# Kernel optimization log

Measured on AMD Instinct MI355X. Metric: run time of the kernel, lower is better.

The kernel has to match this reference:

```python
import jax, jax.numpy as jnp
import numpy as np

N, E, B = 20000, 320000, 64
HID, DEPTH, NFREQ = 128, 4, 8
NODE_DIM, EDGE_DIM, SG = 4, 3, 230
TWO_PI = 2.0 * np.pi


def setup_inputs() -> dict:
    key = jax.random.key(0)
    ks = jax.random.split(key, 20)
    inp = {}
    inp["x"] = jax.random.normal(ks[0], (N, NODE_DIM), jnp.float32)
    inp["edge_index"] = jax.random.randint(ks[1], (2, E), 0, N)
    inp["edge_attr"] = jax.random.normal(ks[2], (E, EDGE_DIM), jnp.float32)
    inp["batch"] = jnp.sort(jax.random.randint(ks[3], (N,), 0, B))
    inp["space_group"] = jax.random.randint(ks[4], (B,), 0, SG)
    inp["node_w"] = jax.random.normal(ks[5], (NODE_DIM, HID), jnp.float32) * 0.1
    inp["node_b"] = jnp.zeros((HID,), jnp.float32)
    inp["sg_table"] = jax.random.normal(ks[6], (SG, HID), jnp.float32) * 0.1
    inp["lin_w"] = jax.random.normal(ks[7], (DEPTH, 2 * HID + EDGE_DIM, HID), jnp.float32) * 0.05
    inp["lin_b"] = jnp.zeros((DEPTH, HID), jnp.float32)
    inp["att_w"] = jax.random.normal(ks[8], (DEPTH, 2 * HID + EDGE_DIM), jnp.float32) * 0.05
    inp["att_b"] = jnp.zeros((DEPTH,), jnp.float32)
    inp["fk_w"] = jax.random.normal(ks[9], (DEPTH, NFREQ, HID, HID), jnp.float32) * 0.1
    inp["fk_b"] = jnp.zeros((DEPTH, HID), jnp.float32)
    inp["bn_g"] = jnp.ones((DEPTH, HID), jnp.float32)
    inp["bn_b"] = jnp.zeros((DEPTH, HID), jnp.float32)
    inp["pool_w"] = jax.random.normal(ks[10], (HID,), jnp.float32) * 0.1
    inp["pool_b"] = jnp.zeros((), jnp.float32)
    inp["head_w1"] = jax.random.normal(ks[11], (4, 2 * HID, HID), jnp.float32) * 0.05
    inp["head_b1"] = jnp.zeros((4, HID), jnp.float32)
    for i, (nm, od) in enumerate([("e", 1), ("s", 3), ("c", 7), ("m", 3)]):
        inp[nm + "_w2"] = jax.random.normal(ks[12 + i], (HID, od), jnp.float32) * 0.05
        inp[nm + "_b2"] = jnp.zeros((od,), jnp.float32)
    return inp


def reference(x, edge_index, edge_attr, batch, space_group, node_w, node_b, sg_table,
              lin_w, lin_b, att_w, att_b, fk_w, fk_b, bn_g, bn_b, pool_w, pool_b,
              head_w1, head_b1, e_w2, e_b2, s_w2, s_b2, c_w2, c_b2, m_w2, m_b2):
    src, dst = edge_index[0], edge_index[1]  # x_j = x[src], x_i = x[dst]
    h = x @ node_w + node_b                  # [N, HID]
    sg = sg_table[space_group]               # [B, HID]
    freqs = jnp.arange(1, NFREQ + 1, dtype=h.dtype)
    for l in range(DEPTH):
        # edge conv: gather-concat-linear-sigmoid attention-scatter add
        tmp = jnp.concatenate([h[dst], h[src], edge_attr], axis=-1)   # [E, 2H+3]
        alpha = jax.nn.sigmoid(tmp @ att_w[l] + att_b[l])[:, None]    # [E, 1]
        msg = alpha * (tmp @ lin_w[l] + lin_b[l])                     # [E, H]
        h_conv = jax.ops.segment_sum(msg, dst, num_segments=N)
        # Fourier-Kolmogorov branch
        ang = TWO_PI * freqs[None, :, None] * h[:, None, :]           # [N, K, H]
        h_fk = (jnp.einsum('nki,kio->no', jnp.sin(ang), fk_w[l])
                + jnp.einsum('nki,kio->no', jnp.cos(ang), fk_w[l]) + fk_b[l])
        h = h_conv + h_fk
        # BatchNorm1d (batch statistics, training semantics) + ReLU; dropout = identity (eval)
        mu = h.mean(axis=0)
        var = h.var(axis=0)
        h = (h - mu) / jnp.sqrt(var + 1e-5) * bn_g[l] + bn_b[l]
        h = jax.nn.relu(h)
    # attention pool: softmax over ALL nodes (dim=0), as in the original
    a = jax.nn.softmax(h @ pool_w + pool_b, axis=0)[:, None]          # [N, 1]
    pooled = jax.ops.segment_sum(a * h, batch, num_segments=B)        # [B, H]
    comb = jnp.concatenate([pooled, sg], axis=-1)                     # [B, 2H]

    def head(i, w2, b2):
        z = jax.nn.relu(comb @ head_w1[i] + head_b1[i])
        return z @ w2 + b2

    energy = head(0, e_w2, e_b2)          # [B, 1]
    stability = head(1, s_w2, s_b2)       # [B, 3]
    crystal_system = head(2, c_w2, c_b2)  # [B, 7]
    material_type = head(3, m_w2, m_b2)   # [B, 3]
    return energy, stability, crystal_system, material_type
```

## Files before the change

### kernel.cpp

```cpp
#include <hip/hip_runtime.h>
#include <math.h>

#define HID 128
#define DEPTH 4
#define PSPLIT 16
#define SMAXB 40

typedef _Float16 half8 __attribute__((ext_vector_type(8)));
typedef float f4 __attribute__((ext_vector_type(4)));

__global__ void k_node_embed(const float* __restrict__ x, const float* __restrict__ nw,
                             const float* __restrict__ nb, float* __restrict__ h, int N) {
    int idx = blockIdx.x * blockDim.x + threadIdx.x;
    if (idx >= N * HID) return;
    int n = idx >> 7, c = idx & 127;
    float acc = nb[c];
#pragma unroll
    for (int d = 0; d < 4; ++d) acc += x[n * 4 + d] * nw[d * HID + c];
    h[idx] = acc;
}

__global__ void k_wsplit(const float* __restrict__ fkw, _Float16* __restrict__ whi,
                         _Float16* __restrict__ wlo) {
    __shared__ float sh[64][65];
    int bid = blockIdx.x;
    int l = bid >> 5; int r = bid & 31; int kb = r >> 1; int nbk = r & 1;
    const float* W = fkw + (size_t)l * 131072;
    _Float16* Hl = whi + (size_t)l * 131072;
    _Float16* Ll = wlo + (size_t)l * 131072;
    int k0 = kb * 64, n0 = nbk * 64;
    for (int i = threadIdx.x; i < 4096; i += 256) {
        int kk = i >> 6, nn = i & 63;
        sh[kk][nn] = W[(k0 + kk) * HID + n0 + nn];
    }
    __syncthreads();
    for (int i = threadIdx.x; i < 4096; i += 256) {
        int nn = i >> 6, kk = i & 63;
        float w = sh[kk][nn];
        _Float16 hi = (_Float16)w;
        _Float16 lo = (_Float16)((w - (float)hi) * 2048.f);
        Hl[(n0 + nn) * 1024 + k0 + kk] = hi;
        Ll[(n0 + nn) * 1024 + k0 + kk] = lo;
    }
}

__global__ void k_hist(const int* __restrict__ dst, int* __restrict__ deg, int E) {
    int e = blockIdx.x * 256 + threadIdx.x;
    if (e < E) atomicAdd(&deg[dst[e]], 1);
}

__global__ void k_scan_a(const int* __restrict__ deg, int* __restrict__ bsum, int N) {
    __shared__ int sh[256];
    int i = blockIdx.x * 256 + threadIdx.x;
    sh[threadIdx.x] = (i < N) ? deg[i] : 0;
    __syncthreads();
    for (int off = 128; off > 0; off >>= 1) {
        if (threadIdx.x < (unsigned)off) sh[threadIdx.x] += sh[threadIdx.x + off];
        __syncthreads();
    }
    if (threadIdx.x == 0) bsum[blockIdx.x] = sh[0];
}

__global__ void k_scan_b(int* __restrict__ bsum, int nb) {
    __shared__ int sh[256];
    int v = (threadIdx.x < (unsigned)nb) ? bsum[threadIdx.x] : 0;
    sh[threadIdx.x] = v;
    __syncthreads();
    for (int off = 1; off < 256; off <<= 1) {
        int add = (threadIdx.x >= (unsigned)off) ? sh[threadIdx.x - off] : 0;
        __syncthreads();
        sh[threadIdx.x] += add;
        __syncthreads();
    }
    if (threadIdx.x < (unsigned)nb) bsum[threadIdx.x] = sh[threadIdx.x] - v;
}

__global__ void k_scan_c(const int* __restrict__ deg, const int* __restrict__ bsum,
                         int* __restrict__ offs, int* __restrict__ cursor, int N) {
    __shared__ int sh[256];
    int i = blockIdx.x * 256 + threadIdx.x;
    int v = (i < N) ? deg[i] : 0;
    sh[threadIdx.x] = v;
    __syncthreads();
    for (int off = 1; off < 256; off <<= 1) {
        int add = (threadIdx.x >= (unsigned)off) ? sh[threadIdx.x - off] : 0;
        __syncthreads();
        sh[threadIdx.x] += add;
        __syncthreads();
    }
    int ex = bsum[blockIdx.x] + sh[threadIdx.x] - v;
    if (i < N) { offs[i] = ex; cursor[i] = ex; }
    if (i == N - 1) offs[N] = ex + v;
}

__global__ void k_scatter(const int* __restrict__ src, const int* __restrict__ dst,
                          const float* __restrict__ ea, int* cursor,
                          int* __restrict__ srco, float4* __restrict__ ea3o, int E) {
    int e = blockIdx.x * 256 + threadIdx.x;
    if (e < E) {
        int d = dst[e];
        int p = atomicAdd(&cursor[d], 1);
        srco[p] = src[e];
        float4 q;
        q.x = ea[e * 3 + 0]; q.y = ea[e * 3 + 1]; q.z = ea[e * 3 + 2]; q.w = 0.f;
        ea3o[p] = q;
    }
}

__global__ void k_bstart(const int* __restrict__ batch, int* __restrict__ boffs, int N, int B) {
    int n = blockIdx.x * 256 + threadIdx.x;
    if (n >= N) return;
    int b1 = batch[n];
    if (n == 0) for (int b = 0; b <= b1; ++b) boffs[b] = 0;
    int b2 = (n + 1 < N) ? batch[n + 1] : B;
    for (int b = b1 + 1; b <= b2; ++b) boffs[b] = n + 1;
}

__global__ __launch_bounds__(256) void k_node_lin(const float* __restrict__ h,
                           const float* __restrict__ linw, const float* __restrict__ linb,
                           const float* __restrict__ attw, const float* __restrict__ attb,
                           float* __restrict__ A1, float* __restrict__ A2,
                           float* __restrict__ a1, float* __restrict__ a2, int N) {
    __shared__ float hT[HID][20];
    int nb = blockIdx.x * 16;
    int tid = threadIdx.x;
    for (int i = tid; i < 16 * HID; i += 256) {
        int n = i >> 7, c = i & 127;
        int gn = nb + n;
        hT[c][n] = (gn < N) ? h[gn * HID + c] : 0.f;
    }
    __syncthreads();
    {
        int node = tid >> 4, lane16 = tid & 15;
        float p1 = 0.f, p2 = 0.f;
#pragma unroll
        for (int j = 0; j < 8; ++j) {
            int k = lane16 * 8 + j;
            float hv = hT[k][node];
            p1 += hv * attw[k];
            p2 += hv * attw[128 + k];
        }
        for (int off = 8; off > 0; off >>= 1) {
            p1 += __shfl_down(p1, off, 16);
            p2 += __shfl_down(p2, off, 16);
        }
        int gn = nb + node;
        if (lane16 == 0 && gn < N) {
            a1[gn] = p1 + attb[0];
            a2[gn] = p2;
        }
    }
    int c = tid & 127, r = tid >> 7;
    const float* Wd = linw;
    const float* Ws = linw + 128 * HID;
    float acc1[8] = {0, 0, 0, 0, 0, 0, 0, 0}, acc2[8] = {0, 0, 0, 0, 0, 0, 0, 0};
#pragma unroll 4
    for (int k = 0; k < HID; ++k) {
        float wd = Wd[k * HID + c];
        float ws = Ws[k * HID + c];
        float4 h0 = *(const float4*)&hT[k][r * 8];
        float4 h1 = *(const float4*)&hT[k][r * 8 + 4];
        acc1[0] += h0.x * wd; acc2[0] += h0.x * ws;
        acc1[1] += h0.y * wd; acc2[1] += h0.y * ws;
        acc1[2] += h0.z * wd; acc2[2] += h0.z * ws;
        acc1[3] += h0.w * wd; acc2[3] += h0.w * ws;
        acc1[4] += h1.x * wd; acc2[4] += h1.x * ws;
        acc1[5] += h1.y * wd; acc2[5] += h1.y * ws;
        acc1[6] += h1.z * wd; acc2[6] += h1.z * ws;
        acc1[7] += h1.w * wd; acc2[7] += h1.w * ws;
    }
    float lb = linb[c];
#pragma unroll
    for (int j = 0; j < 8; ++j) {
        int gn = nb + r * 8 + j;
        if (gn < N) {
            A1[(size_t)gn * HID + c] = acc1[j] + lb;
            A2[(size_t)gn * HID + c] = acc2[j];
        }
    }
}

__global__ __launch_bounds__(256) void k_edge(const float* __restrict__ A1,
        const float* __restrict__ A2, const float* __restrict__ a1,
        const float* __restrict__ a2, const int* __restrict__ srco,
        const float4* __restrict__ ea3o, const int* __restrict__ offs,
        const float* __restrict__ linw3, const float* __restrict__ attw3,
        float* __restrict__ hconv, double* __restrict__ stats, int N) {
    __shared__ float part[8][HID + 4];
    int n = blockIdx.x;
    int tid = threadIdx.x;
    if (n == 0) stats[tid] = 0.0;
    int lane32 = tid & 31, slot = tid >> 5;
    int c4 = lane32 * 4;
    float4 w0v = *(const float4*)&linw3[c4];
    float4 w1v = *(const float4*)&linw3[HID + c4];
    float4 w2v = *(const float4*)&linw3[2 * HID + c4];
    float aw0 = attw3[0], aw1 = attw3[1], aw2 = attw3[2];
    float a1n = a1[n];
    float4 A1v = *(const float4*)&A1[(size_t)n * HID + c4];
    float4 acc; acc.x = acc.y = acc.z = acc.w = 0.f;
    int s0 = offs[n], s1 = offs[n + 1];
    for (int idx = s0 + slot; idx < s1; idx += 8) {
        int s = srco[idx];
        float4 q = ea3o[idx];
        float logit = a1n + a2[s] + q.x * aw0 + q.y * aw1 + q.z * aw2;
        float al = 1.f / (1.f + __expf(-logit));
        float4 a2v = *(const float4*)&A2[(size_t)s * HID + c4];
        float4 pre;
        pre.x = A1v.x + a2v.x + q.x * w0v.x + q.y * w1v.x + q.z * w2v.x;
        pre.y = A1v.y + a2v.y + q.x * w0v.y + q.y * w1v.y + q.z * w2v.y;
        pre.z = A1v.z + a2v.z + q.x * w0v.z + q.y * w1v.z + q.z * w2v.z;
        pre.w = A1v.w + a2v.w + q.x * w0v.w + q.y * w1v.w + q.z * w2v.w;
        acc.x += al * pre.x; acc.y += al * pre.y;
        acc.z += al * pre.z; acc.w += al * pre.w;
    }
    *(float4*)&part[slot][c4] = acc;
    __syncthreads();
    if (slot == 0) {
        float4 p = *(const float4*)&part[0][c4];
#pragma unroll
        for (int s = 1; s < 8; ++s) {
            float4 r = *(const float4*)&part[s][c4];
            p.x += r.x; p.y += r.y; p.z += r.z; p.w += r.w;
        }
        *(float4*)&hconv[(size_t)n * HID + c4] = p;
    }
}

#define FK_ROWS 32
__global__ __launch_bounds__(512, 4) void k_fk(const float* __restrict__ h,
        const _Float16* __restrict__ whi, const _Float16* __restrict__ wlo,
        float* __restrict__ p0, float* __restrict__ p1, int N) {
    __shared__ _Float16 ahi[FK_ROWS * 256];
    __shared__ _Float16 alo[FK_ROWS * 256];
    int tid = threadIdx.x;
    int bx = blockIdx.x;
    int nb = (bx >> 1) * FK_ROWS;
    int ks = bx & 1;
    int row = tid >> 4;
    int o16 = tid & 15;
    {
    }
    int gn = nb + row;
    int rc = (gn < N) ? gn : (N - 1);
    const float* hp = h + (size_t)rc * HID + o16 * 8;
    float hv[8];
    *(float4*)&hv[0] = *(const float4*)hp;
    *(float4*)&hv[4] = *(const float4*)(hp + 4);
    int rs = row & 7;
    int lane = tid & 63, wv = tid >> 6;
    int quad = lane >> 4, l16 = lane & 15;
    int n0w = wv * 16;
    int rs16 = (l16 & 7) << 3;
    f4 acc0[2], accL[2];
#pragma unroll
    for (int mi = 0; mi < 2; ++mi) { acc0[mi] = (f4)(0.f); accL[mi] = (f4)(0.f); }
    int kbase0 = ks * 512;
#pragma unroll
    for (int chunk = 0; chunk < 2; ++chunk) {
        int kbase = kbase0 + chunk * 256;
        int fr0 = kbase >> 7;
#pragma unroll
        for (int g = 0; g < 2; ++g) {
            float freqf = 6.2831853f * (float)(fr0 + g + 1);
            half8 vh, vl;
#pragma unroll
            for (int j = 0; j < 8; ++j) {
                float ang = freqf * hv[j] + 0.78539816f;
                float a = 1.41421356f * __sinf(ang);
                _Float16 hi = (_Float16)a;
                vh[j] = hi;
                vl[j] = (_Float16)((a - (float)hi) * 2048.f);
            }
            int oct = (g * 16 + o16) ^ rs;
            *(half8*)&ahi[row * 256 + oct * 8] = vh;
            *(half8*)&alo[row * 256 + oct * 8] = vl;
        }
        __syncthreads();
        const _Float16* bhp = whi + (size_t)(n0w + l16) * 1024 + kbase + quad * 8;
        const _Float16* blp = wlo + (size_t)(n0w + l16) * 1024 + kbase + quad * 8;
#pragma unroll 2
        for (int step = 0; step < 8; ++step) {
            int ka = (step * 32 + quad * 8) ^ rs16;
            int ko = step * 32;
            half8 bh = *(const half8*)(bhp + ko);
            half8 bl = *(const half8*)(blp + ko);
            half8 ah[2], al[2];
#pragma unroll
            for (int mi = 0; mi < 2; ++mi) {
                ah[mi] = *(const half8*)&ahi[(l16 + mi * 16) * 256 + ka];
                al[mi] = *(const half8*)&alo[(l16 + mi * 16) * 256 + ka];
            }
#pragma unroll
            for (int mi = 0; mi < 2; ++mi) {
                acc0[mi] = __builtin_amdgcn_mfma_f32_16x16x32_f16(ah[mi], bh, acc0[mi], 0, 0, 0);
                accL[mi] = __builtin_amdgcn_mfma_f32_16x16x32_f16(ah[mi], bl, accL[mi], 0, 0, 0);
                accL[mi] = __builtin_amdgcn_mfma_f32_16x16x32_f16(al[mi], bh, accL[mi], 0, 0, 0);
            }
        }
        __syncthreads();
    }
    float* p = ks ? p1 : p0;
    const float inv = 1.0f / 2048.0f;
#pragma unroll
    for (int mi = 0; mi < 2; ++mi)
#pragma unroll
        for (int r = 0; r < 4; ++r) {
            int g2 = nb + mi * 16 + quad * 4 + r;
            if (g2 < N)
                p[g2 * HID + n0w + l16] = acc0[mi][r] + accL[mi][r] * inv;
        }
}

__global__ __launch_bounds__(256) void k_bn_stats(float* __restrict__ hconv,
                           const float* __restrict__ p0, const float* __restrict__ p1,
                           const float* __restrict__ fkb,
                           double* __restrict__ stats, int N) {
    int tid = threadIdx.x;
    int cq = tid & 31, rg = tid >> 5;
    int c4 = cq * 4;
    float4 bias = *(const float4*)&fkb[c4];
    float s1[4] = {0, 0, 0, 0}, s2[4] = {0, 0, 0, 0};
    for (int n = blockIdx.x * 8 + rg; n < N; n += gridDim.x * 8) {
        size_t idx = (size_t)n * HID + c4;
        float4 a  = *(const float4*)&hconv[idx];
        float4 b0 = *(const float4*)&p0[idx];
        float4 b1 = *(const float4*)&p1[idx];
        float4 v;
        v.x = a.x + b0.x + b1.x + bias.x;
        v.y = a.y + b0.y + b1.y + bias.y;
        v.z = a.z + b0.z + b1.z + bias.z;
        v.w = a.w + b0.w + b1.w + bias.w;
        *(float4*)&hconv[idx] = v;
        s1[0] += v.x; s2[0] += v.x * v.x;
        s1[1] += v.y; s2[1] += v.y * v.y;
        s1[2] += v.z; s2[2] += v.z * v.z;
        s1[3] += v.w; s2[3] += v.w * v.w;
    }
#pragma unroll
    for (int j = 0; j < 4; ++j) {
        s1[j] += __shfl_down(s1[j], 32);
        s2[j] += __shfl_down(s2[j], 32);
    }
    __shared__ float sh1[4][32][4], sh2[4][32][4];
    int wv = tid >> 6, lane = tid & 63;
    if (lane < 32) {
#pragma unroll
        for (int j = 0; j < 4; ++j) { sh1[wv][lane][j] = s1[j]; sh2[wv][lane][j] = s2[j]; }
    }
    __syncthreads();
    if (tid < 128) {
        int cq2 = tid >> 2, j2 = tid & 3;
        float t1 = sh1[0][cq2][j2] + sh1[1][cq2][j2] + sh1[2][cq2][j2] + sh1[3][cq2][j2];
        float t2 = sh2[0][cq2][j2] + sh2[1][cq2][j2] + sh2[2][cq2][j2] + sh2[3][cq2][j2];
        int c = cq2 * 4 + j2;
        atomicAdd(&stats[c], (double)t1);
        atomicAdd(&stats[128 + c], (double)t2);
    }
}

__global__ void k_bn_apply(const float* __restrict__ hsum, const double* __restrict__ stats,
                           const float* __restrict__ g, const float* __restrict__ b,
                           const float* __restrict__ pw, const float* __restrict__ pb,
                           float* __restrict__ h, float* __restrict__ s,
                           int do_score, int N) {
    int idx = blockIdx.x * 256 + threadIdx.x;
    int row = idx >> 5, cq = idx & 31;
    int c4 = cq * 4;
    int valid = row < N;
    double invN = 1.0 / (double)N;
    float p = 0.f;
    if (valid) {
        float4 hv = *(const float4*)&hsum[(size_t)row * HID + c4];
        float vin[4] = {hv.x, hv.y, hv.z, hv.w};
        float4 ov;
        float* po = &ov.x;
#pragma unroll
        for (int j = 0; j < 4; ++j) {
            int c = c4 + j;
            float mu = (float)(stats[c] * invN);
            float var = (float)(stats[128 + c] * invN) - mu * mu;
            float inv = 1.f / sqrtf(var + 1e-5f);
            float sc = g[c] * inv;
            float sh = b[c] - mu * sc;
            float oo = fmaxf(vin[j] * sc + sh, 0.f);
            po[j] = oo;
            if (do_score) p += oo * pw[c];
        }
        *(float4*)&h[(size_t)row * HID + c4] = ov;
    }
    if (do_score) {
        for (int off = 16; off > 0; off >>= 1) p += __shfl_down(p, off, 32);
        if ((threadIdx.x & 31) == 0 && valid) s[row] = p + pb[0];
    }
}

__global__ void k_smax1(const float* __restrict__ s, float* __restrict__ mzp, int N) {
    __shared__ float red[256];
    float m = -INFINITY;
    for (int n = blockIdx.x * 256 + threadIdx.x; n < N; n += SMAXB * 256)
        m = fmaxf(m, s[n]);
    red[threadIdx.x] = m;
    __syncthreads();
    for (int off = 128; off > 0; off >>= 1) {
        if (threadIdx.x < (unsigned)off)
            red[threadIdx.x] = fmaxf(red[threadIdx.x], red[threadIdx.x + off]);
        __syncthreads();
    }
    m = red[0];
    __syncthreads();
    float z = 0.f;
    for (int n = blockIdx.x * 256 + threadIdx.x; n < N; n += SMAXB * 256)
        z += __expf(s[n] - m);
    red[threadIdx.x] = z;
    __syncthreads();
    for (int off = 128; off > 0; off >>= 1) {
        if (threadIdx.x < (unsigned)off) red[threadIdx.x] += red[threadIdx.x + off];
        __syncthreads();
    }
    if (threadIdx.x == 0) { mzp[blockIdx.x * 2] = m; mzp[blockIdx.x * 2 + 1] = red[0]; }
}

__device__ __forceinline__ void combine_mz(const float* mzp, float& m, float& Z) {
    m = -INFINITY;
#pragma unroll 8
    for (int i = 0; i < SMAXB; ++i) m = fmaxf(m, mzp[i * 2]);
    Z = 0.f;
#pragma unroll 8
    for (int i = 0; i < SMAXB; ++i) Z += mzp[i * 2 + 1] * __expf(mzp[i * 2] - m);
}

__global__ void k_pool_part(const float* __restrict__ h, const float* __restrict__ s,
                            const float* __restrict__ mzp, const int* __restrict__ boffs,
                            float* __restrict__ part) {
    int b = blockIdx.x >> 4, split = blockIdx.x & (PSPLIT - 1);
    int c = threadIdx.x & 127, half = threadIdx.x >> 7;
    float m, Z;
    combine_mz(mzp, m, Z);
    (void)Z;
    int n0 = boffs[b], n1 = boffs[b + 1];
    float acc = 0.f;
    for (int n = n0 + split * 2 + half; n < n1; n += PSPLIT * 2)
        acc += __expf(s[n] - m) * h[n * HID + c];
    __shared__ float prt[2][HID];
    prt[half][c] = acc;
    __syncthreads();
    if (half == 0) part[(size_t)(b * PSPLIT + split) * HID + c] = prt[0][c] + prt[1][c];
}

__global__ void k_pool_sum(const float* __restrict__ part, const float* __restrict__ mzp,
                           float* __restrict__ pooled) {
    int b = blockIdx.x, c = threadIdx.x;
    float m, Z;
    combine_mz(mzp, m, Z);
    float acc = 0.f;
#pragma unroll
    for (int i = 0; i < PSPLIT; ++i) acc += part[(size_t)(b * PSPLIT + i) * HID + c];
    pooled[b * HID + c] = acc / Z;
}

__global__ __launch_bounds__(256) void k_head(const float* __restrict__ pooled,
                       const float* __restrict__ sg_table,
                       const int* __restrict__ space_group,
                       const float* __restrict__ hw1, const float* __restrict__ hb1,
                       const float* __restrict__ ew2, const float* __restrict__ eb2,
                       const float* __restrict__ sw2, const float* __restrict__ sb2,
                       const float* __restrict__ cw2, const float* __restrict__ cb2,
                       const float* __restrict__ mw2, const float* __restrict__ mb2,
                       float* __restrict__ out, int B) {
    __shared__ float comb[256];
    __shared__ float zred[2][128];
    __shared__ float zsh[128];
    int b = blockIdx.x >> 2, i = blockIdx.x & 3;
    int t = threadIdx.x;
    comb[t] = (t < 128) ? pooled[b * HID + t] : sg_table[space_group[b] * HID + (t - 128)];
    __syncthreads();
    int half = t >> 7, tt = t & 127;
    const float* W = hw1 + ((size_t)i * 256 + half * 128) * HID;
    const float* cb = &comb[half * 128];
    float z = 0.f;
#pragma unroll 8
    for (int k = 0; k < 128; ++k) z += cb[k] * W[k * HID + tt];
    zred[half][tt] = z;
    __syncthreads();
    if (t < 128) zsh[t] = fmaxf(zred[0][t] + zred[1][t] + hb1[i * HID + t], 0.f);
    __syncthreads();
    const int od[4] = {1, 3, 7, 3};
    const int base[4] = {0, 64, 256, 704};
    const float* w2 = (i == 0) ? ew2 : (i == 1) ? sw2 : (i == 2) ? cw2 : mw2;
    const float* b2 = (i == 0) ? eb2 : (i == 1) ? sb2 : (i == 2) ? cb2 : mb2;
    int odi = od[i];
    if (t < odi) {
        float o = b2[t];
        for (int c = 0; c < HID; ++c) o += zsh[c] * w2[c * odi + t];
        out[base[i] + b * odi + t] = o;
    }
}

extern "C" void kernel_launch(void* const* d_in, const int* in_sizes, int n_in,
                              void* d_out, int out_size, void* d_ws, size_t ws_size,
                              hipStream_t stream) {
    const float* x          = (const float*)d_in[0];
    const int*   edge_index = (const int*)d_in[1];
    const float* edge_attr  = (const float*)d_in[2];
    const int*   batch      = (const int*)d_in[3];
    const int*   space_group= (const int*)d_in[4];
    const float* node_w     = (const float*)d_in[5];
    const float* node_b     = (const float*)d_in[6];
    const float* sg_table   = (const float*)d_in[7];
    const float* lin_w      = (const float*)d_in[8];
    const float* lin_b      = (const float*)d_in[9];
    const float* att_w      = (const float*)d_in[10];
    const float* att_b      = (const float*)d_in[11];
    const float* fk_w       = (const float*)d_in[12];
    const float* fk_b       = (const float*)d_in[13];
    const float* bn_g       = (const float*)d_in[14];
    const float* bn_b       = (const float*)d_in[15];
    const float* pool_w     = (const float*)d_in[16];
    const float* pool_b     = (const float*)d_in[17];
    const float* head_w1    = (const float*)d_in[18];
    const float* head_b1    = (const float*)d_in[19];
    const float* ew2 = (const float*)d_in[20]; const float* eb2 = (const float*)d_in[21];
    const float* sw2 = (const float*)d_in[22]; const float* sb2 = (const float*)d_in[23];
    const float* cw2 = (const float*)d_in[24]; const float* cb2 = (const float*)d_in[25];
    const float* mw2 = (const float*)d_in[26]; const float* mb2 = (const float*)d_in[27];
    float* out = (float*)d_out;

    const int N = in_sizes[3];
    const int E = in_sizes[1] / 2;
    const int B = in_sizes[4];
    const int* src = edge_index;
    const int* dst = edge_index + E;

    char* w = (char*)d_ws;
    auto alloc = [&](size_t bytes) { char* p = w; w += (bytes + 255) & ~(size_t)255; return p; };
    float*  h      = (float*)alloc((size_t)N * HID * 4);
    float*  A1     = (float*)alloc((size_t)N * HID * 4);
    float*  A2     = (float*)alloc((size_t)N * HID * 4);
    float*  hconv  = (float*)alloc((size_t)N * HID * 4);
    float*  a1     = (float*)alloc((size_t)N * 4);
    float*  a2     = (float*)alloc((size_t)N * 4);
    float*  sbuf   = (float*)alloc((size_t)N * 4);
    int*    deg    = (int*)alloc((size_t)N * 4);
    int*    cursor = (int*)alloc((size_t)N * 4);
    int*    offs   = (int*)alloc((size_t)(N + 1) * 4);
    int*    srco   = (int*)alloc((size_t)E * 4);
    float4* ea3o   = (float4*)alloc((size_t)E * 16);
    _Float16* whi  = (_Float16*)alloc((size_t)DEPTH * 1024 * HID * 2);
    _Float16* wlo  = (_Float16*)alloc((size_t)DEPTH * 1024 * HID * 2);
    int*    bsum   = (int*)alloc(256 * 4);
    int*    boffs  = (int*)alloc((size_t)(B + 1) * 4);
    double* stats  = (double*)alloc(256 * 8);
    float*  mzp    = (float*)alloc(SMAXB * 2 * 4);
    float*  part   = (float*)alloc((size_t)B * PSPLIT * HID * 4);
    float*  pooled = (float*)alloc((size_t)B * HID * 4);

    const int nchunk = (N + 255) / 256;
    const int echunk = (E + 255) / 256;

    k_wsplit<<<128, 256, 0, stream>>>(fk_w, whi, wlo);
    hipMemsetAsync(deg, 0, (size_t)N * 4, stream);
    k_hist<<<echunk, 256, 0, stream>>>(dst, deg, E);
    k_scan_a<<<nchunk, 256, 0, stream>>>(deg, bsum, N);
    k_scan_b<<<1, 256, 0, stream>>>(bsum, nchunk);
    k_scan_c<<<nchunk, 256, 0, stream>>>(deg, bsum, offs, cursor, N);
    k_scatter<<<echunk, 256, 0, stream>>>(src, dst, edge_attr, cursor, srco, ea3o, E);
    k_bstart<<<nchunk, 256, 0, stream>>>(batch, boffs, N, B);

    k_node_embed<<<(N * HID + 255) / 256, 256, 0, stream>>>(x, node_w, node_b, h, N);

    for (int l = 0; l < DEPTH; ++l) {
        const float* linw_l = lin_w + (size_t)l * 259 * HID;
        k_node_lin<<<(N + 15) / 16, 256, 0, stream>>>(
            h, linw_l, lin_b + l * HID, att_w + (size_t)l * 259, att_b + l,
            A1, A2, a1, a2, N);
        k_edge<<<N, 256, 0, stream>>>(A1, A2, a1, a2, srco, ea3o, offs,
                                      linw_l + 256 * HID, att_w + (size_t)l * 259 + 256,
                                      hconv, stats, N);
        k_fk<<<((N + FK_ROWS - 1) / FK_ROWS) * 2, 512, 0, stream>>>(
            h, whi + (size_t)l * 131072, wlo + (size_t)l * 131072, A1, A2, N);
        k_bn_stats<<<320, 256, 0, stream>>>(hconv, A1, A2, fk_b + l * HID, stats, N);
        k_bn_apply<<<(N * 32 + 255) / 256, 256, 0, stream>>>(
            hconv, stats, bn_g + l * HID, bn_b + l * HID, pool_w, pool_b,
            h, sbuf, (l == DEPTH - 1) ? 1 : 0, N);
    }

    k_smax1<<<SMAXB, 256, 0, stream>>>(sbuf, mzp, N);
    k_pool_part<<<B * PSPLIT, 256, 0, stream>>>(h, sbuf, mzp, boffs, part);
    k_pool_sum<<<B, 128, 0, stream>>>(part, mzp, pooled);
    k_head<<<B * 4, 256, 0, stream>>>(pooled, sg_table, space_group, head_w1, head_b1,
                                      ew2, eb2, sw2, sb2, cw2, cb2, mw2, mb2, out, B);
}
```

Before: 709.8 us.

## Merge k-split fk blocks into one double-buffered pipelined kernel

Each k_fk block now processes the full K=1024 reduction instead of two blocks writing separate partial outputs. The sin/cos activation tile for the next chunk is generated into a second LDS buffer while MFMAs consume the current one. This removes one partial buffer's global write and read in the BN stats kernel and overlaps trig with matrix math. It doubles LDS per block and halves the grid, which may lower occupancy and parallelism.

```diff
diff --git a/kernel.cpp b/kernel.cpp
--- a/kernel.cpp
+++ b/kernel.cpp
@@ -230,17 +230,13 @@
 #define FK_ROWS 32
 __global__ __launch_bounds__(512, 4) void k_fk(const float* __restrict__ h,
         const _Float16* __restrict__ whi, const _Float16* __restrict__ wlo,
-        float* __restrict__ p0, float* __restrict__ p1, int N) {
-    __shared__ _Float16 ahi[FK_ROWS * 256];
-    __shared__ _Float16 alo[FK_ROWS * 256];
+        float* __restrict__ p0, int N) {
+    __shared__ _Float16 ahi[2][FK_ROWS * 256];
+    __shared__ _Float16 alo[2][FK_ROWS * 256];
     int tid = threadIdx.x;
-    int bx = blockIdx.x;
-    int nb = (bx >> 1) * FK_ROWS;
-    int ks = bx & 1;
+    int nb = blockIdx.x * FK_ROWS;
     int row = tid >> 4;
     int o16 = tid & 15;
-    {
-    }
     int gn = nb + row;
     int rc = (gn < N) ? gn : (N - 1);
     const float* hp = h + (size_t)rc * HID + o16 * 8;
@@ -255,11 +251,8 @@
     f4 acc0[2], accL[2];
 #pragma unroll
     for (int mi = 0; mi < 2; ++mi) { acc0[mi] = (f4)(0.f); accL[mi] = (f4)(0.f); }
-    int kbase0 = ks * 512;
-#pragma unroll
-    for (int chunk = 0; chunk < 2; ++chunk) {
-        int kbase = kbase0 + chunk * 256;
-        int fr0 = kbase >> 7;
+
+    auto trig = [&](int fr0, int buf) {
 #pragma unroll
         for (int g = 0; g < 2; ++g) {
             float freqf = 6.2831853f * (float)(fr0 + g + 1);
@@ -273,10 +266,18 @@
                 vl[j] = (_Float16)((a - (float)hi) * 2048.f);
             }
             int oct = (g * 16 + o16) ^ rs;
-            *(half8*)&ahi[row * 256 + oct * 8] = vh;
-            *(half8*)&alo[row * 256 + oct * 8] = vl;
-        }
-        __syncthreads();
+            *(half8*)&ahi[buf][row * 256 + oct * 8] = vh;
+            *(half8*)&alo[buf][row * 256 + oct * 8] = vl;
+        }
+    };
+
+    trig(0, 0);
+    __syncthreads();
+#pragma unroll
+    for (int c = 0; c < 4; ++c) {
+        int cb = c & 1;
+        if (c < 3) trig((c + 1) * 2, (c + 1) & 1);
+        int kbase = c * 256;
         const _Float16* bhp = whi + (size_t)(n0w + l16) * 1024 + kbase + quad * 8;
         const _Float16* blp = wlo + (size_t)(n0w + l16) * 1024 + kbase + quad * 8;
 #pragma unroll 2
@@ -288,8 +289,8 @@
             half8 ah[2], al[2];
 #pragma unroll
             for (int mi = 0; mi < 2; ++mi) {
-                ah[mi] = *(const half8*)&ahi[(l16 + mi * 16) * 256 + ka];
-                al[mi] = *(const half8*)&alo[(l16 + mi * 16) * 256 + ka];
+                ah[mi] = *(const half8*)&ahi[cb][(l16 + mi * 16) * 256 + ka];
+                al[mi] = *(const half8*)&alo[cb][(l16 + mi * 16) * 256 + ka];
             }
 #pragma unroll
             for (int mi = 0; mi < 2; ++mi) {
@@ -300,7 +301,6 @@
         }
         __syncthreads();
     }
-    float* p = ks ? p1 : p0;
     const float inv = 1.0f / 2048.0f;
 #pragma unroll
     for (int mi = 0; mi < 2; ++mi)
@@ -308,12 +308,12 @@
         for (int r = 0; r < 4; ++r) {
             int g2 = nb + mi * 16 + quad * 4 + r;
             if (g2 < N)
-                p[g2 * HID + n0w + l16] = acc0[mi][r] + accL[mi][r] * inv;
+                p0[g2 * HID + n0w + l16] = acc0[mi][r] + accL[mi][r] * inv;
         }
 }
 
 __global__ __launch_bounds__(256) void k_bn_stats(float* __restrict__ hconv,
-                           const float* __restrict__ p0, const float* __restrict__ p1,
+                           const float* __restrict__ p0,
                            const float* __restrict__ fkb,
                            double* __restrict__ stats, int N) {
     int tid = threadIdx.x;
@@ -325,12 +325,11 @@
         size_t idx = (size_t)n * HID + c4;
         float4 a  = *(const float4*)&hconv[idx];
         float4 b0 = *(const float4*)&p0[idx];
-        float4 b1 = *(const float4*)&p1[idx];
         float4 v;
-        v.x = a.x + b0.x + b1.x + bias.x;
-        v.y = a.y + b0.y + b1.y + bias.y;
-        v.z = a.z + b0.z + b1.z + bias.z;
-        v.w = a.w + b0.w + b1.w + bias.w;
+        v.x = a.x + b0.x + bias.x;
+        v.y = a.y + b0.y + bias.y;
+        v.z = a.z + b0.z + bias.z;
+        v.w = a.w + b0.w + bias.w;
         *(float4*)&hconv[idx] = v;
         s1[0] += v.x; s2[0] += v.x * v.x;
         s1[1] += v.y; s2[1] += v.y * v.y;
@@ -577,9 +576,9 @@
         k_edge<<<N, 256, 0, stream>>>(A1, A2, a1, a2, srco, ea3o, offs,
                                       linw_l + 256 * HID, att_w + (size_t)l * 259 + 256,
                                       hconv, stats, N);
-        k_fk<<<((N + FK_ROWS - 1) / FK_ROWS) * 2, 512, 0, stream>>>(
-            h, whi + (size_t)l * 131072, wlo + (size_t)l * 131072, A1, A2, N);
-        k_bn_stats<<<320, 256, 0, stream>>>(hconv, A1, A2, fk_b + l * HID, stats, N);
+        k_fk<<<(N + FK_ROWS - 1) / FK_ROWS, 512, 0, stream>>>(
+            h, whi + (size_t)l * 131072, wlo + (size_t)l * 131072, A1, N);
+        k_bn_stats<<<320, 256, 0, stream>>>(hconv, A1, fk_b + l * HID, stats, N);
         k_bn_apply<<<(N * 32 + 255) / 256, 256, 0, stream>>>(
             hconv, stats, bn_g + l * HID, bn_b + l * HID, pool_w, pool_b,
             h, sbuf, (l == DEPTH - 1) ? 1 : 0, N);
```

Result: slower. 724.6 us (+2.1%).
